# Kernel tuning notes

Hardware: AMD Instinct MI355X
Metric: run time of the kernel (lower is better)

Reference implementation:

```python
import jax, jax.numpy as jnp
import numpy as np

D_MODEL, D_K, D_V, H = 64, 32, 32, 8
B, HH, WW = 2, 48, 48
NQ = HH * WW


def setup_inputs() -> dict:
    key = jax.random.key(0)
    ks = jax.random.split(key, 16)
    inp = {
        "queries": jax.random.normal(ks[0], (B, D_MODEL, HH, WW), jnp.float32),
        "keys": jax.random.normal(ks[1], (B, D_MODEL, HH, WW), jnp.float32),
        "values": jax.random.normal(ks[2], (B, D_MODEL, HH, WW), jnp.float32),
        "attention_weights": jax.random.uniform(ks[3], (B, H, NQ, NQ), jnp.float32),
        "attention_mask": jax.random.randint(ks[4], (B, H, NQ, NQ), 0, 2) > 0,
        # Linear params: torch init normal(std=0.001) weights, zero bias
        "Wq": 0.001 * jax.random.normal(ks[5], (H * D_K, D_MODEL), jnp.float32),
        "bq": jnp.zeros((H * D_K,), jnp.float32),
        "Wk": 0.001 * jax.random.normal(ks[6], (H * D_K, D_MODEL), jnp.float32),
        "bk": jnp.zeros((H * D_K,), jnp.float32),
        "Wv": 0.001 * jax.random.normal(ks[7], (H * D_V, D_MODEL), jnp.float32),
        "bv": jnp.zeros((H * D_V,), jnp.float32),
        "Wo": 0.001 * jax.random.normal(ks[8], (D_MODEL, H * D_V), jnp.float32),
        "bo": jnp.zeros((D_MODEL,), jnp.float32),
    }
    return inp


def reference(queries, keys, values, attention_weights, attention_mask,
              Wq, bq, Wk, bk, Wv, bv, Wo, bo):
    b, c, hh, ww = queries.shape
    nq = hh * ww
    # torch .view(b, -1, c) on contiguous (b,c,h,w) is a raw row-major reshape
    qf = queries.reshape(b, nq, c)
    kf = keys.reshape(b, nq, c)
    vf = values.reshape(b, nq, c)
    q = (qf @ Wq.T + bq).reshape(b, nq, H, D_K).transpose(0, 2, 1, 3)  # b h nq dk
    k = (kf @ Wk.T + bk).reshape(b, nq, H, D_K).transpose(0, 2, 1, 3)  # b h nk dk
    v = (vf @ Wv.T + bv).reshape(b, nq, H, D_V).transpose(0, 2, 1, 3)  # b h nk dv
    att = jnp.einsum('bhqd,bhkd->bhqk', q, k) / np.sqrt(D_K).astype(np.float32)
    att = att * attention_weights
    att = jnp.where(attention_mask, -jnp.inf, att)
    att = jax.nn.softmax(att, axis=-1)  # dropout is identity in eval mode
    out = jnp.einsum('bhqk,bhkd->bhqd', att, v)
    out = out.transpose(0, 2, 1, 3).reshape(b, nq, H * D_V)
    out = out @ Wo.T + bo  # (b, nq, d_model)
    return out.reshape(b, -1, hh, ww)  # (b, d_model, h, w)
```

## Files before the change

### kernel.cpp

```cpp
#include <hip/hip_runtime.h>


typedef __attribute__((ext_vector_type(8))) short bf16x8;
typedef __attribute__((ext_vector_type(4))) short bf16x4;
typedef __attribute__((ext_vector_type(4))) float f32x4;
typedef __attribute__((ext_vector_type(4))) unsigned int u32x4;

constexpr int B_  = 2;
constexpr int H_  = 8;
constexpr int NQ_ = 2304;
constexpr int DM_ = 64;
constexpr int DK_ = 32;
constexpr int NT_ = NQ_ / 32;
constexpr int CH_ = 3;
constexpr int TPC_ = NT_ / CH_;
constexpr int GT_ = B_ * H_ * (NQ_ / 16);
constexpr float SCALE_ = 0.17677669529663687f;

constexpr size_t OFF_Q    = 0;
constexpr size_t OFF_K    = 2359296;
constexpr size_t OFF_V    = 4718592;
constexpr size_t OFF_OMID = 7077888;
constexpr size_t OFF_FLAG = 11796480;
constexpr size_t OFF_OP   = 11796736;
constexpr size_t OFF_ML   = 25952512;

static __device__ __forceinline__ unsigned short f2bf(float f) {
    unsigned int u = __builtin_bit_cast(unsigned int, f);
    u += 0x7fffu + ((u >> 16) & 1u);
    return (unsigned short)(u >> 16);
}

__global__ void detect_mask_k(const unsigned int* __restrict__ m, int* __restrict__ flag) {
    int t = threadIdx.x;
    unsigned int v = 0;
    for (int k = 0; k < 16; ++k) v |= m[t * 16 + k];
    unsigned long long b = __ballot(v > 1u);
    if (t == 0) *flag = (b != 0ull) ? 1 : 0;
}

__global__ __launch_bounds__(256) void proj_qkv_k(
    const float* __restrict__ qin, const float* __restrict__ kin, const float* __restrict__ vin,
    const float* __restrict__ Wq, const float* __restrict__ bq,
    const float* __restrict__ Wk, const float* __restrict__ bk,
    const float* __restrict__ Wv, const float* __restrict__ bv,
    unsigned short* __restrict__ Qbf, unsigned short* __restrict__ Kbf,
    unsigned short* __restrict__ Vbf)
{
    const int sel = blockIdx.y;
    const float* in  = sel == 0 ? qin : (sel == 1 ? kin : vin);
    const float* W   = sel == 0 ? Wq  : (sel == 1 ? Wk  : Wv);
    const float* bia = sel == 0 ? bq  : (sel == 1 ? bk  : bv);

    const int rt = blockIdx.x;
    const int b  = rt / (NQ_ / 8);
    const int r0 = (rt % (NQ_ / 8)) * 8;

    __shared__ alignas(16) float ins[8][64];
    const int t = threadIdx.x;
    const float4* src = reinterpret_cast<const float4*>(in + ((size_t)b * NQ_ + r0) * DM_);
    if (t < 128) reinterpret_cast<float4*>(&ins[0][0])[t] = src[t];
    __syncthreads();

    float acc[8];
#pragma unroll
    for (int r = 0; r < 8; ++r) acc[r] = 0.f;
    const float* wrow = W + t * DM_;
    for (int m = 0; m < DM_; ++m) {
        float wv = wrow[m];
#pragma unroll
        for (int r = 0; r < 8; ++r) acc[r] += ins[r][m] * wv;
    }
    const float bb = bia[t];
    const int h = t >> 5, d = t & 31;
#pragma unroll
    for (int r = 0; r < 8; ++r) {
        float o = acc[r] + bb;
        if (sel == 0) o *= SCALE_;
        unsigned short bvv = f2bf(o);
        if (sel == 2) Vbf[(((size_t)b * H_ + h) * DK_ + d) * NQ_ + (r0 + r)] = bvv;
        else {
            unsigned short* out = (sel == 1) ? Kbf : Qbf;
            out[(((size_t)b * H_ + h) * NQ_ + (r0 + r)) * DK_ + d] = bvv;
        }
    }
}

struct Slot {
    bf16x8 ka0, ka1;
    f32x4  w0, w1;
    bf16x4 v00, v01, v10, v11;
};
template<bool ISBYTE> struct MaskSlot;
template<> struct MaskSlot<true>  { unsigned int a, b; };
template<> struct MaskSlot<false> { u32x4 a, b; };

template<bool ISBYTE>
static __device__ __forceinline__ void issue_slot(
    Slot& s, MaskSlot<ISBYTE>& ms,
    const unsigned short* __restrict__ kbase, const unsigned short* __restrict__ vbase,
    const float* __restrict__ wrow, const unsigned char* __restrict__ mrowp,
    int j0, int l15, int hi)
{
    s.ka0 = *reinterpret_cast<const bf16x8*>(kbase + (size_t)(j0 + l15) * DK_ + 8 * hi);
    s.ka1 = *reinterpret_cast<const bf16x8*>(kbase + (size_t)(j0 + 16 + l15) * DK_ + 8 * hi);
    s.w0  = *reinterpret_cast<const f32x4*>(wrow + j0 + 4 * hi);
    s.w1  = *reinterpret_cast<const f32x4*>(wrow + j0 + 16 + 4 * hi);
    if constexpr (ISBYTE) {
        ms.a = *reinterpret_cast<const unsigned int*>(mrowp + j0 + 4 * hi);
        ms.b = *reinterpret_cast<const unsigned int*>(mrowp + j0 + 16 + 4 * hi);
    } else {
        ms.a = *reinterpret_cast<const u32x4*>(mrowp + (size_t)(j0 + 4 * hi) * 4);
        ms.b = *reinterpret_cast<const u32x4*>(mrowp + (size_t)(j0 + 16 + 4 * hi) * 4);
    }
    s.v00 = *reinterpret_cast<const bf16x4*>(vbase + (size_t)l15 * NQ_ + j0 + 4 * hi);
    s.v01 = *reinterpret_cast<const bf16x4*>(vbase + (size_t)l15 * NQ_ + j0 + 16 + 4 * hi);
    s.v10 = *reinterpret_cast<const bf16x4*>(vbase + (size_t)(16 + l15) * NQ_ + j0 + 4 * hi);
    s.v11 = *reinterpret_cast<const bf16x4*>(vbase + (size_t)(16 + l15) * NQ_ + j0 + 16 + 4 * hi);
}

template<bool ISBYTE>
static __device__ __forceinline__ void consume_slot(
    const Slot& s, const MaskSlot<ISBYTE>& ms, bf16x8 qb,
    f32x4& oacc0, f32x4& oacc1, float& lrun)
{
    const f32x4 zero = {0.f, 0.f, 0.f, 0.f};
    f32x4 s0 = __builtin_amdgcn_mfma_f32_16x16x32_bf16(s.ka0, qb, zero, 0, 0, 0);
    f32x4 s1 = __builtin_amdgcn_mfma_f32_16x16x32_bf16(s.ka1, qb, zero, 0, 0, 0);

    unsigned int ba, bb;
    if constexpr (ISBYTE) { ba = ms.a; bb = ms.b; }
    else {
        ba = (ms.a[0] & 1u) | ((ms.a[1] & 1u) << 8) | ((ms.a[2] & 1u) << 16) | ((ms.a[3] & 1u) << 24);
        bb = (ms.b[0] & 1u) | ((ms.b[1] & 1u) << 8) | ((ms.b[2] & 1u) << 16) | ((ms.b[3] & 1u) << 24);
    }

    float p0[4], p1[4];
#pragma unroll
    for (int r = 0; r < 4; ++r) {
        float e0 = __expf(s0[r] * s.w0[r]);
        float e1 = __expf(s1[r] * s.w1[r]);
        p0[r] = ((ba >> (8 * r)) & 0xffu) ? 0.f : e0;
        p1[r] = ((bb >> (8 * r)) & 0xffu) ? 0.f : e1;
    }
    lrun += ((p0[0] + p0[1]) + (p0[2] + p0[3])) + ((p1[0] + p1[1]) + (p1[2] + p1[3]));

    bf16x8 pa;
#pragma unroll
    for (int r = 0; r < 4; ++r) {
        pa[r]     = (short)f2bf(p0[r]);
        pa[4 + r] = (short)f2bf(p1[r]);
    }
    bf16x8 vb0 = __builtin_shufflevector(s.v00, s.v01, 0, 1, 2, 3, 4, 5, 6, 7);
    bf16x8 vb1 = __builtin_shufflevector(s.v10, s.v11, 0, 1, 2, 3, 4, 5, 6, 7);
    oacc0 = __builtin_amdgcn_mfma_f32_16x16x32_bf16(pa, vb0, oacc0, 0, 0, 0);
    oacc1 = __builtin_amdgcn_mfma_f32_16x16x32_bf16(pa, vb1, oacc1, 0, 0, 0);
}

template<bool ISBYTE>
__global__ __launch_bounds__(256) void attn_k(
    const unsigned short* __restrict__ Qbf,
    const unsigned short* __restrict__ Kbf,
    const unsigned short* __restrict__ Vbf,
    const float* __restrict__ attw,
    const unsigned char* __restrict__ maskb,
    const int* __restrict__ flagp,
    float* __restrict__ Opart,
    float* __restrict__ MLpart)
{
    if (((*flagp) != 0) != ISBYTE) return;

    const int lane = threadIdx.x & 63;
    const int l15 = lane & 15, hi = lane >> 4;
    const int g = blockIdx.x * 4 + (threadIdx.x >> 6);
    const int chunk = blockIdx.y;
    const int bh = g / (NQ_ / 16);
    const int it = g % (NQ_ / 16);
    const int i0 = it * 16;

    const unsigned short* qbase = Qbf + (size_t)bh * NQ_ * DK_;
    const unsigned short* kbase = Kbf + (size_t)bh * NQ_ * DK_;
    const unsigned short* vbase = Vbf + (size_t)bh * DK_ * NQ_;

    const int q = i0 + l15;
    bf16x8 qb = *reinterpret_cast<const bf16x8*>(qbase + (size_t)q * DK_ + 8 * hi);

    const float* wrow = attw + ((size_t)bh * NQ_ + q) * NQ_;
    const unsigned char* mrowp = maskb + ((size_t)bh * NQ_ + q) * NQ_ * (ISBYTE ? 1 : 4);

    f32x4 oacc0 = {0.f, 0.f, 0.f, 0.f}, oacc1 = {0.f, 0.f, 0.f, 0.f};
    float lrun = 0.f;

    const int t0 = chunk * TPC_, t1 = t0 + TPC_;

    Slot sl0, sl1, sl2;
    MaskSlot<ISBYTE> ms0, ms1, ms2;
    issue_slot<ISBYTE>(sl0, ms0, kbase, vbase, wrow, mrowp, t0 * 32, l15, hi);
    issue_slot<ISBYTE>(sl1, ms1, kbase, vbase, wrow, mrowp, (t0 + 1) * 32, l15, hi);
    issue_slot<ISBYTE>(sl2, ms2, kbase, vbase, wrow, mrowp, (t0 + 2) * 32, l15, hi);

    for (int tt = t0; tt < t1; tt += 3) {
        consume_slot<ISBYTE>(sl0, ms0, qb, oacc0, oacc1, lrun);
        if (tt + 3 < t1)
            issue_slot<ISBYTE>(sl0, ms0, kbase, vbase, wrow, mrowp, (tt + 3) * 32, l15, hi);
        consume_slot<ISBYTE>(sl1, ms1, qb, oacc0, oacc1, lrun);
        if (tt + 4 < t1)
            issue_slot<ISBYTE>(sl1, ms1, kbase, vbase, wrow, mrowp, (tt + 4) * 32, l15, hi);
        consume_slot<ISBYTE>(sl2, ms2, qb, oacc0, oacc1, lrun);
        if (tt + 5 < t1)
            issue_slot<ISBYTE>(sl2, ms2, kbase, vbase, wrow, mrowp, (tt + 5) * 32, l15, hi);
    }

    float* op = Opart + ((size_t)chunk * GT_ + g) * 512;
#pragma unroll
    for (int r = 0; r < 4; ++r) {
        op[(4 * hi + r) * 32 + l15]      = oacc0[r];
        op[(4 * hi + r) * 32 + 16 + l15] = oacc1[r];
    }
    lrun += __shfl_xor(lrun, 16, 64);
    lrun += __shfl_xor(lrun, 32, 64);
    if (hi == 0) {
        float* mlp = MLpart + ((size_t)chunk * GT_ + g) * 32;
        mlp[l15] = lrun;
    }
}

__global__ __launch_bounds__(64) void combine_k(
    const float* __restrict__ Opart, const float* __restrict__ MLpart,
    float* __restrict__ Omid)
{
    const int g = blockIdx.x;
    const int lane = threadIdx.x;
    const int row = lane >> 2;
    const int c4  = (lane & 3) * 8;
    const int bh = g / (NQ_ / 16);
    const int it = g % (NQ_ / 16);
    const int b = bh / H_, h = bh % H_;

    float lg = 0.f;
#pragma unroll
    for (int c = 0; c < CH_; ++c)
        lg += MLpart[((size_t)c * GT_ + g) * 32 + row];
    float inv = 1.0f / lg;

    const size_t ob = (size_t)row * 32 + c4;
    f32x4 a0 = {0.f,0.f,0.f,0.f}, a1 = {0.f,0.f,0.f,0.f};
#pragma unroll
    for (int c = 0; c < CH_; ++c) {
        const float* opp = Opart + ((size_t)c * GT_ + g) * 512 + ob;
        a0 += *reinterpret_cast<const f32x4*>(opp);
        a1 += *reinterpret_cast<const f32x4*>(opp + 4);
    }
    a0 *= inv; a1 *= inv;
    float* dst = Omid + ((size_t)b * NQ_ + it * 16 + row) * 256 + h * 32 + c4;
    *reinterpret_cast<f32x4*>(dst)     = a0;
    *reinterpret_cast<f32x4*>(dst + 4) = a1;
}

__global__ __launch_bounds__(256) void proj_out_k(
    const float* __restrict__ Omid, const float* __restrict__ Wo,
    const float* __restrict__ bo, float* __restrict__ out)
{
    const int rt = blockIdx.x;
    const int b  = rt / (NQ_ / 16);
    const int r0 = (rt % (NQ_ / 16)) * 16;

    __shared__ alignas(16) float lds[16][256];
    const int t = threadIdx.x;
    const float4* src = reinterpret_cast<const float4*>(Omid + ((size_t)b * NQ_ + r0) * 256);
#pragma unroll
    for (int k = 0; k < 4; ++k) reinterpret_cast<float4*>(&lds[0][0])[t + k * 256] = src[t + k * 256];
    __syncthreads();

    const int m = t & 63, rg = t >> 6;
    float acc[4] = {0.f, 0.f, 0.f, 0.f};
    const float* wrow = Wo + m * 256;
    for (int c = 0; c < 256; ++c) {
        float wv = wrow[c];
#pragma unroll
        for (int rr = 0; rr < 4; ++rr) acc[rr] += lds[rg * 4 + rr][c] * wv;
    }
    const float bb = bo[m];
#pragma unroll
    for (int rr = 0; rr < 4; ++rr)
        out[((size_t)b * NQ_ + r0 + rg * 4 + rr) * 64 + m] = acc[rr] + bb;
}

extern "C" void kernel_launch(void* const* d_in, const int* in_sizes, int n_in,
                              void* d_out, int out_size, void* d_ws, size_t ws_size,
                              hipStream_t stream)
{
    (void)in_sizes; (void)n_in; (void)out_size; (void)ws_size;
    const float* qin  = (const float*)d_in[0];
    const float* kin  = (const float*)d_in[1];
    const float* vin  = (const float*)d_in[2];
    const float* attw = (const float*)d_in[3];
    const void*  mask = d_in[4];
    const float* Wq = (const float*)d_in[5];
    const float* bq = (const float*)d_in[6];
    const float* Wk = (const float*)d_in[7];
    const float* bk = (const float*)d_in[8];
    const float* Wv = (const float*)d_in[9];
    const float* bv = (const float*)d_in[10];
    const float* Wo = (const float*)d_in[11];
    const float* bo = (const float*)d_in[12];

    char* ws = (char*)d_ws;
    unsigned short* Qbf   = (unsigned short*)(ws + OFF_Q);
    unsigned short* Kbf   = (unsigned short*)(ws + OFF_K);
    unsigned short* Vbf   = (unsigned short*)(ws + OFF_V);
    float*          Omid  = (float*)(ws + OFF_OMID);
    int*            flag  = (int*)(ws + OFF_FLAG);
    float*          Opart = (float*)(ws + OFF_OP);
    float*          MLp   = (float*)(ws + OFF_ML);

    detect_mask_k<<<1, 64, 0, stream>>>((const unsigned int*)mask, flag);
    proj_qkv_k<<<dim3(B_ * NQ_ / 8, 3), 256, 0, stream>>>(
        qin, kin, vin, Wq, bq, Wk, bk, Wv, bv, Qbf, Kbf, Vbf);
    attn_k<true><<<dim3(GT_ / 4, CH_), 256, 0, stream>>>(
        Qbf, Kbf, Vbf, attw, (const unsigned char*)mask, flag, Opart, MLp);
    attn_k<false><<<dim3(GT_ / 4, CH_), 256, 0, stream>>>(
        Qbf, Kbf, Vbf, attw, (const unsigned char*)mask, flag, Opart, MLp);
    combine_k<<<GT_, 64, 0, stream>>>(Opart, MLp, Omid);
    proj_out_k<<<B_ * NQ_ / 16, 256, 0, stream>>>(Omid, Wo, bo, (float*)d_out);
}
```

Baseline: 241.4 us.

## Prefetch attention weights and mask in 4-tile spans, separate from K/V pipeline

Restructures the attention streaming loop so the dominant attention-weight and mask loads are fetched in larger 4-tile spans, double-buffered (WA/WB, MA/MB) well ahead of use. K/V loads move to their own two-slot ring. The two mask variants are also split into separate kernels with different launch_bounds occupancy hints (3 and 2 blocks per CU). The aim is more memory-level parallelism on the bandwidth-bound weight/mask stream. The cost is higher register pressure, and the loop now hardcodes 24 tiles per chunk.

```diff
diff --git a/kernel.cpp b/kernel.cpp
--- a/kernel.cpp
+++ b/kernel.cpp
@@ -86,60 +86,71 @@
     }
 }
 
-struct Slot {
+struct KVSlot {
     bf16x8 ka0, ka1;
-    f32x4  w0, w1;
     bf16x4 v00, v01, v10, v11;
 };
-template<bool ISBYTE> struct MaskSlot;
-template<> struct MaskSlot<true>  { unsigned int a, b; };
-template<> struct MaskSlot<false> { u32x4 a, b; };
-
-template<bool ISBYTE>
-static __device__ __forceinline__ void issue_slot(
-    Slot& s, MaskSlot<ISBYTE>& ms,
+
+static __device__ __forceinline__ void issue_kv(KVSlot& s,
     const unsigned short* __restrict__ kbase, const unsigned short* __restrict__ vbase,
-    const float* __restrict__ wrow, const unsigned char* __restrict__ mrowp,
     int j0, int l15, int hi)
 {
     s.ka0 = *reinterpret_cast<const bf16x8*>(kbase + (size_t)(j0 + l15) * DK_ + 8 * hi);
     s.ka1 = *reinterpret_cast<const bf16x8*>(kbase + (size_t)(j0 + 16 + l15) * DK_ + 8 * hi);
-    s.w0  = *reinterpret_cast<const f32x4*>(wrow + j0 + 4 * hi);
-    s.w1  = *reinterpret_cast<const f32x4*>(wrow + j0 + 16 + 4 * hi);
-    if constexpr (ISBYTE) {
-        ms.a = *reinterpret_cast<const unsigned int*>(mrowp + j0 + 4 * hi);
-        ms.b = *reinterpret_cast<const unsigned int*>(mrowp + j0 + 16 + 4 * hi);
-    } else {
-        ms.a = *reinterpret_cast<const u32x4*>(mrowp + (size_t)(j0 + 4 * hi) * 4);
-        ms.b = *reinterpret_cast<const u32x4*>(mrowp + (size_t)(j0 + 16 + 4 * hi) * 4);
-    }
     s.v00 = *reinterpret_cast<const bf16x4*>(vbase + (size_t)l15 * NQ_ + j0 + 4 * hi);
     s.v01 = *reinterpret_cast<const bf16x4*>(vbase + (size_t)l15 * NQ_ + j0 + 16 + 4 * hi);
     s.v10 = *reinterpret_cast<const bf16x4*>(vbase + (size_t)(16 + l15) * NQ_ + j0 + 4 * hi);
     s.v11 = *reinterpret_cast<const bf16x4*>(vbase + (size_t)(16 + l15) * NQ_ + j0 + 16 + 4 * hi);
 }
 
-template<bool ISBYTE>
-static __device__ __forceinline__ void consume_slot(
-    const Slot& s, const MaskSlot<ISBYTE>& ms, bf16x8 qb,
+template<bool ISBYTE> struct MSpan;
+template<> struct MSpan<true>  { unsigned int m[8]; };
+template<> struct MSpan<false> { u32x4 m[8]; };
+
+static __device__ __forceinline__ void loadW(f32x4 (&W)[8], const float* __restrict__ p) {
+#pragma unroll
+    for (int u = 0; u < 4; ++u) {
+        W[2 * u]     = *reinterpret_cast<const f32x4*>(p + 32 * u);
+        W[2 * u + 1] = *reinterpret_cast<const f32x4*>(p + 32 * u + 16);
+    }
+}
+
+static __device__ __forceinline__ void loadM(MSpan<true>& M, const unsigned char* __restrict__ p) {
+#pragma unroll
+    for (int u = 0; u < 4; ++u) {
+        M.m[2 * u]     = *reinterpret_cast<const unsigned int*>(p + 32 * u);
+        M.m[2 * u + 1] = *reinterpret_cast<const unsigned int*>(p + 32 * u + 16);
+    }
+}
+static __device__ __forceinline__ void loadM(MSpan<false>& M, const unsigned char* __restrict__ p) {
+#pragma unroll
+    for (int u = 0; u < 4; ++u) {
+        M.m[2 * u]     = *reinterpret_cast<const u32x4*>(p + 128 * u);
+        M.m[2 * u + 1] = *reinterpret_cast<const u32x4*>(p + 128 * u + 64);
+    }
+}
+
+static __device__ __forceinline__ unsigned int mb32(unsigned int v) { return v; }
+static __device__ __forceinline__ unsigned int mb32(u32x4 v) {
+    return (v[0] & 1u) | ((v[1] & 1u) << 8) | ((v[2] & 1u) << 16) | ((v[3] & 1u) << 24);
+}
+
+template<typename MT>
+static __device__ __forceinline__ void consume_tile(
+    const KVSlot& s, f32x4 w0, f32x4 w1, MT m0r, MT m1r, bf16x8 qb,
     f32x4& oacc0, f32x4& oacc1, float& lrun)
 {
     const f32x4 zero = {0.f, 0.f, 0.f, 0.f};
     f32x4 s0 = __builtin_amdgcn_mfma_f32_16x16x32_bf16(s.ka0, qb, zero, 0, 0, 0);
     f32x4 s1 = __builtin_amdgcn_mfma_f32_16x16x32_bf16(s.ka1, qb, zero, 0, 0, 0);
 
-    unsigned int ba, bb;
-    if constexpr (ISBYTE) { ba = ms.a; bb = ms.b; }
-    else {
-        ba = (ms.a[0] & 1u) | ((ms.a[1] & 1u) << 8) | ((ms.a[2] & 1u) << 16) | ((ms.a[3] & 1u) << 24);
-        bb = (ms.b[0] & 1u) | ((ms.b[1] & 1u) << 8) | ((ms.b[2] & 1u) << 16) | ((ms.b[3] & 1u) << 24);
-    }
+    const unsigned int ba = mb32(m0r), bb = mb32(m1r);
 
     float p0[4], p1[4];
 #pragma unroll
     for (int r = 0; r < 4; ++r) {
-        float e0 = __expf(s0[r] * s.w0[r]);
-        float e1 = __expf(s1[r] * s.w1[r]);
+        float e0 = __expf(s0[r] * w0[r]);
+        float e1 = __expf(s1[r] * w1[r]);
         p0[r] = ((ba >> (8 * r)) & 0xffu) ? 0.f : e0;
         p1[r] = ((bb >> (8 * r)) & 0xffu) ? 0.f : e1;
     }
@@ -158,7 +169,24 @@
 }
 
 template<bool ISBYTE>
-__global__ __launch_bounds__(256) void attn_k(
+static __device__ __forceinline__ void consume4(
+    KVSlot& sA, KVSlot& sB, const f32x4 (&W)[8], const MSpan<ISBYTE>& M,
+    int tb, int t1,
+    const unsigned short* __restrict__ kbase, const unsigned short* __restrict__ vbase,
+    int l15, int hi, bf16x8 qb, f32x4& o0, f32x4& o1, float& lr)
+{
+    consume_tile(sA, W[0], W[1], M.m[0], M.m[1], qb, o0, o1, lr);
+    if (tb + 2 < t1) issue_kv(sA, kbase, vbase, (tb + 2) * 32, l15, hi);
+    consume_tile(sB, W[2], W[3], M.m[2], M.m[3], qb, o0, o1, lr);
+    if (tb + 3 < t1) issue_kv(sB, kbase, vbase, (tb + 3) * 32, l15, hi);
+    consume_tile(sA, W[4], W[5], M.m[4], M.m[5], qb, o0, o1, lr);
+    if (tb + 4 < t1) issue_kv(sA, kbase, vbase, (tb + 4) * 32, l15, hi);
+    consume_tile(sB, W[6], W[7], M.m[6], M.m[7], qb, o0, o1, lr);
+    if (tb + 5 < t1) issue_kv(sB, kbase, vbase, (tb + 5) * 32, l15, hi);
+}
+
+template<bool ISBYTE>
+static __device__ __forceinline__ void attn_body(
     const unsigned short* __restrict__ Qbf,
     const unsigned short* __restrict__ Kbf,
     const unsigned short* __restrict__ Vbf,
@@ -185,30 +213,38 @@
     const int q = i0 + l15;
     bf16x8 qb = *reinterpret_cast<const bf16x8*>(qbase + (size_t)q * DK_ + 8 * hi);
 
-    const float* wrow = attw + ((size_t)bh * NQ_ + q) * NQ_;
-    const unsigned char* mrowp = maskb + ((size_t)bh * NQ_ + q) * NQ_ * (ISBYTE ? 1 : 4);
+    const float* wl = attw + ((size_t)bh * NQ_ + q) * NQ_ + 4 * hi;
+    const unsigned char* ml = maskb + (((size_t)bh * NQ_ + q) * NQ_ + 4 * hi) * (ISBYTE ? 1 : 4);
+
+    const int t0 = chunk * TPC_, t1 = t0 + TPC_;
+    const size_t msc = ISBYTE ? 1 : 4;
+
+    f32x4 WA[8], WB[8];
+    MSpan<ISBYTE> MA, MB;
+    KVSlot sA, sB;
+
+    loadW(WA, wl + (size_t)t0 * 32);
+    loadM(MA, ml + (size_t)t0 * 32 * msc);
+    loadW(WB, wl + (size_t)t0 * 32 + 128);
+    loadM(MB, ml + ((size_t)t0 * 32 + 128) * msc);
+    issue_kv(sA, kbase, vbase, t0 * 32, l15, hi);
+    issue_kv(sB, kbase, vbase, t0 * 32 + 32, l15, hi);
 
     f32x4 oacc0 = {0.f, 0.f, 0.f, 0.f}, oacc1 = {0.f, 0.f, 0.f, 0.f};
     float lrun = 0.f;
 
-    const int t0 = chunk * TPC_, t1 = t0 + TPC_;
-
-    Slot sl0, sl1, sl2;
-    MaskSlot<ISBYTE> ms0, ms1, ms2;
-    issue_slot<ISBYTE>(sl0, ms0, kbase, vbase, wrow, mrowp, t0 * 32, l15, hi);
-    issue_slot<ISBYTE>(sl1, ms1, kbase, vbase, wrow, mrowp, (t0 + 1) * 32, l15, hi);
-    issue_slot<ISBYTE>(sl2, ms2, kbase, vbase, wrow, mrowp, (t0 + 2) * 32, l15, hi);
-
-    for (int tt = t0; tt < t1; tt += 3) {
-        consume_slot<ISBYTE>(sl0, ms0, qb, oacc0, oacc1, lrun);
-        if (tt + 3 < t1)
-            issue_slot<ISBYTE>(sl0, ms0, kbase, vbase, wrow, mrowp, (tt + 3) * 32, l15, hi);
-        consume_slot<ISBYTE>(sl1, ms1, qb, oacc0, oacc1, lrun);
-        if (tt + 4 < t1)
-            issue_slot<ISBYTE>(sl1, ms1, kbase, vbase, wrow, mrowp, (tt + 4) * 32, l15, hi);
-        consume_slot<ISBYTE>(sl2, ms2, qb, oacc0, oacc1, lrun);
-        if (tt + 5 < t1)
-            issue_slot<ISBYTE>(sl2, ms2, kbase, vbase, wrow, mrowp, (tt + 5) * 32, l15, hi);
+    for (int sp = 0; sp < 3; ++sp) {
+        const int tb = t0 + 8 * sp;
+        consume4<ISBYTE>(sA, sB, WA, MA, tb, t1, kbase, vbase, l15, hi, qb, oacc0, oacc1, lrun);
+        if (sp < 2) {
+            loadW(WA, wl + (size_t)(tb + 8) * 32);
+            loadM(MA, ml + (size_t)(tb + 8) * 32 * msc);
+        }
+        consume4<ISBYTE>(sA, sB, WB, MB, tb + 4, t1, kbase, vbase, l15, hi, qb, oacc0, oacc1, lrun);
+        if (sp < 2) {
+            loadW(WB, wl + (size_t)(tb + 12) * 32);
+            loadM(MB, ml + (size_t)(tb + 12) * 32 * msc);
+        }
     }
 
     float* op = Opart + ((size_t)chunk * GT_ + g) * 512;
@@ -223,6 +259,24 @@
         float* mlp = MLpart + ((size_t)chunk * GT_ + g) * 32;
         mlp[l15] = lrun;
     }
+}
+
+__global__ __launch_bounds__(256, 3) void attn_byte_k(
+    const unsigned short* __restrict__ Qbf, const unsigned short* __restrict__ Kbf,
+    const unsigned short* __restrict__ Vbf, const float* __restrict__ attw,
+    const unsigned char* __restrict__ maskb, const int* __restrict__ flagp,
+    float* __restrict__ Opart, float* __restrict__ MLpart)
+{
+    attn_body<true>(Qbf, Kbf, Vbf, attw, maskb, flagp, Opart, MLpart);
+}
+
+__global__ __launch_bounds__(256, 2) void attn_int_k(
+    const unsigned short* __restrict__ Qbf, const unsigned short* __restrict__ Kbf,
+    const unsigned short* __restrict__ Vbf, const float* __restrict__ attw,
+    const unsigned char* __restrict__ maskb, const int* __restrict__ flagp,
+    float* __restrict__ Opart, float* __restrict__ MLpart)
+{
+    attn_body<false>(Qbf, Kbf, Vbf, attw, maskb, flagp, Opart, MLpart);
 }
 
 __global__ __launch_bounds__(64) void combine_k(
@@ -317,9 +371,9 @@
     detect_mask_k<<<1, 64, 0, stream>>>((const unsigned int*)mask, flag);
     proj_qkv_k<<<dim3(B_ * NQ_ / 8, 3), 256, 0, stream>>>(
         qin, kin, vin, Wq, bq, Wk, bk, Wv, bv, Qbf, Kbf, Vbf);
-    attn_k<true><<<dim3(GT_ / 4, CH_), 256, 0, stream>>>(
+    attn_byte_k<<<dim3(GT_ / 4, CH_), 256, 0, stream>>>(
         Qbf, Kbf, Vbf, attw, (const unsigned char*)mask, flag, Opart, MLp);
-    attn_k<false><<<dim3(GT_ / 4, CH_), 256, 0, stream>>>(
+    attn_int_k<<<dim3(GT_ / 4, CH_), 256, 0, stream>>>(
         Qbf, Kbf, Vbf, attw, (const unsigned char*)mask, flag, Opart, MLp);
     combine_k<<<GT_, 64, 0, stream>>>(Opart, MLp, Omid);
     proj_out_k<<<B_ * NQ_ / 16, 256, 0, stream>>>(Omid, Wo, bo, (float*)d_out);
```

New measurement: 241.0 us. No clear change (-0.1%).

## Stage attention weight, mask, K and V tiles into LDS via async global-to-LDS loads

Applied to the files above, without the earlier changes.

The attention kernel now copies the attention-weight rows, int mask rows, K and V tiles straight from global memory into per-wave XOR-swizzled LDS buffers with global_load_lds. It double-buffers them and uses explicit vmcnt waits, replacing the old three-slot register prefetch. Blocks shrink from four waves to three so the grid divides evenly, and each wave gets 16 KB of LDS. The aim is coalesced row-wise streaming of the large weight and mask tensors with less register pressure. The cost is hand-counted waitcnt values and swizzle indexing that must match the load count exactly.

```diff
diff --git a/kernel.cpp b/kernel.cpp
--- a/kernel.cpp
+++ b/kernel.cpp
@@ -31,6 +31,10 @@
     return (unsigned short)(u >> 16);
 }
 
+#define GLL16(SRC, DST) __builtin_amdgcn_global_load_lds( \
+    (const __attribute__((address_space(1))) unsigned int*)(const void*)(SRC), \
+    (__attribute__((address_space(3))) unsigned int*)(void*)(DST), 16, 0, 0)
+
 __global__ void detect_mask_k(const unsigned int* __restrict__ m, int* __restrict__ flag) {
     int t = threadIdx.x;
     unsigned int v = 0;
@@ -86,79 +90,16 @@
     }
 }
 
-struct Slot {
+
+struct Frag {
+    f32x4 w0, w1;
+    u32x4 m0, m1;
     bf16x8 ka0, ka1;
-    f32x4  w0, w1;
     bf16x4 v00, v01, v10, v11;
 };
-template<bool ISBYTE> struct MaskSlot;
-template<> struct MaskSlot<true>  { unsigned int a, b; };
-template<> struct MaskSlot<false> { u32x4 a, b; };
 
 template<bool ISBYTE>
-static __device__ __forceinline__ void issue_slot(
-    Slot& s, MaskSlot<ISBYTE>& ms,
-    const unsigned short* __restrict__ kbase, const unsigned short* __restrict__ vbase,
-    const float* __restrict__ wrow, const unsigned char* __restrict__ mrowp,
-    int j0, int l15, int hi)
-{
-    s.ka0 = *reinterpret_cast<const bf16x8*>(kbase + (size_t)(j0 + l15) * DK_ + 8 * hi);
-    s.ka1 = *reinterpret_cast<const bf16x8*>(kbase + (size_t)(j0 + 16 + l15) * DK_ + 8 * hi);
-    s.w0  = *reinterpret_cast<const f32x4*>(wrow + j0 + 4 * hi);
-    s.w1  = *reinterpret_cast<const f32x4*>(wrow + j0 + 16 + 4 * hi);
-    if constexpr (ISBYTE) {
-        ms.a = *reinterpret_cast<const unsigned int*>(mrowp + j0 + 4 * hi);
-        ms.b = *reinterpret_cast<const unsigned int*>(mrowp + j0 + 16 + 4 * hi);
-    } else {
-        ms.a = *reinterpret_cast<const u32x4*>(mrowp + (size_t)(j0 + 4 * hi) * 4);
-        ms.b = *reinterpret_cast<const u32x4*>(mrowp + (size_t)(j0 + 16 + 4 * hi) * 4);
-    }
-    s.v00 = *reinterpret_cast<const bf16x4*>(vbase + (size_t)l15 * NQ_ + j0 + 4 * hi);
-    s.v01 = *reinterpret_cast<const bf16x4*>(vbase + (size_t)l15 * NQ_ + j0 + 16 + 4 * hi);
-    s.v10 = *reinterpret_cast<const bf16x4*>(vbase + (size_t)(16 + l15) * NQ_ + j0 + 4 * hi);
-    s.v11 = *reinterpret_cast<const bf16x4*>(vbase + (size_t)(16 + l15) * NQ_ + j0 + 16 + 4 * hi);
-}
-
-template<bool ISBYTE>
-static __device__ __forceinline__ void consume_slot(
-    const Slot& s, const MaskSlot<ISBYTE>& ms, bf16x8 qb,
-    f32x4& oacc0, f32x4& oacc1, float& lrun)
-{
-    const f32x4 zero = {0.f, 0.f, 0.f, 0.f};
-    f32x4 s0 = __builtin_amdgcn_mfma_f32_16x16x32_bf16(s.ka0, qb, zero, 0, 0, 0);
-    f32x4 s1 = __builtin_amdgcn_mfma_f32_16x16x32_bf16(s.ka1, qb, zero, 0, 0, 0);
-
-    unsigned int ba, bb;
-    if constexpr (ISBYTE) { ba = ms.a; bb = ms.b; }
-    else {
-        ba = (ms.a[0] & 1u) | ((ms.a[1] & 1u) << 8) | ((ms.a[2] & 1u) << 16) | ((ms.a[3] & 1u) << 24);
-        bb = (ms.b[0] & 1u) | ((ms.b[1] & 1u) << 8) | ((ms.b[2] & 1u) << 16) | ((ms.b[3] & 1u) << 24);
-    }
-
-    float p0[4], p1[4];
-#pragma unroll
-    for (int r = 0; r < 4; ++r) {
-        float e0 = __expf(s0[r] * s.w0[r]);
-        float e1 = __expf(s1[r] * s.w1[r]);
-        p0[r] = ((ba >> (8 * r)) & 0xffu) ? 0.f : e0;
-        p1[r] = ((bb >> (8 * r)) & 0xffu) ? 0.f : e1;
-    }
-    lrun += ((p0[0] + p0[1]) + (p0[2] + p0[3])) + ((p1[0] + p1[1]) + (p1[2] + p1[3]));
-
-    bf16x8 pa;
-#pragma unroll
-    for (int r = 0; r < 4; ++r) {
-        pa[r]     = (short)f2bf(p0[r]);
-        pa[4 + r] = (short)f2bf(p1[r]);
-    }
-    bf16x8 vb0 = __builtin_shufflevector(s.v00, s.v01, 0, 1, 2, 3, 4, 5, 6, 7);
-    bf16x8 vb1 = __builtin_shufflevector(s.v10, s.v11, 0, 1, 2, 3, 4, 5, 6, 7);
-    oacc0 = __builtin_amdgcn_mfma_f32_16x16x32_bf16(pa, vb0, oacc0, 0, 0, 0);
-    oacc1 = __builtin_amdgcn_mfma_f32_16x16x32_bf16(pa, vb1, oacc1, 0, 0, 0);
-}
-
-template<bool ISBYTE>
-__global__ __launch_bounds__(256) void attn_k(
+static __device__ __forceinline__ void attn_body(
     const unsigned short* __restrict__ Qbf,
     const unsigned short* __restrict__ Kbf,
     const unsigned short* __restrict__ Vbf,
@@ -166,49 +107,152 @@
     const unsigned char* __restrict__ maskb,
     const int* __restrict__ flagp,
     float* __restrict__ Opart,
-    float* __restrict__ MLpart)
+    float* __restrict__ MLpart,
+    char* lds)
 {
     if (((*flagp) != 0) != ISBYTE) return;
 
-    const int lane = threadIdx.x & 63;
+    const int tid = threadIdx.x;
+    const int wid = tid >> 6, lane = tid & 63;
     const int l15 = lane & 15, hi = lane >> 4;
-    const int g = blockIdx.x * 4 + (threadIdx.x >> 6);
+    const int g = blockIdx.x * 3 + wid;
     const int chunk = blockIdx.y;
     const int bh = g / (NQ_ / 16);
     const int it = g % (NQ_ / 16);
     const int i0 = it * 16;
+    const int q = i0 + l15;
 
     const unsigned short* qbase = Qbf + (size_t)bh * NQ_ * DK_;
     const unsigned short* kbase = Kbf + (size_t)bh * NQ_ * DK_;
     const unsigned short* vbase = Vbf + (size_t)bh * DK_ * NQ_;
-
-    const int q = i0 + l15;
+    const float* wbase = attw + (size_t)bh * NQ_ * NQ_;
+
     bf16x8 qb = *reinterpret_cast<const bf16x8*>(qbase + (size_t)q * DK_ + 8 * hi);
 
-    const float* wrow = attw + ((size_t)bh * NQ_ + q) * NQ_;
-    const unsigned char* mrowp = maskb + ((size_t)bh * NQ_ + q) * NQ_ * (ISBYTE ? 1 : 4);
+    const int r8 = lane >> 3, q8 = lane & 7;
+    const int wq = (q8 ^ r8) * 4;
+    const float* pW0 = wbase + (size_t)(i0 + r8) * NQ_ + wq;
+    const float* pW1 = pW0 + (size_t)8 * NQ_;
+    const int* pM0 = (const int*)maskb + (size_t)(bh * NQ_ + i0 + r8) * NQ_ + wq;
+    const int* pM1 = pM0 + (size_t)8 * NQ_;
+    const int r4 = lane >> 2, q4 = lane & 3;
+    const int kq = (q4 ^ ((r4 >> 1) & 3)) * 8;
+    const unsigned short* pK0 = kbase + (size_t)r4 * DK_ + kq;
+    const unsigned short* pK1 = pK0 + (size_t)16 * DK_;
+    const unsigned short* pV0 = vbase + (size_t)r4 * NQ_ + kq;
+    const unsigned short* pV1 = pV0 + (size_t)16 * NQ_;
+
+    const unsigned char* mrow = maskb + ((size_t)bh * NQ_ + q) * NQ_;
+
+    char* sb0 = lds + wid * 16384;
+    char* sb1 = sb0 + 8192;
+
+    auto stage = [&](char* sb, int tile) {
+        const int j0 = tile * 32;
+        GLL16(pW0 + j0, sb);
+        GLL16(pW1 + j0, sb + 1024);
+        if constexpr (!ISBYTE) {
+            GLL16(pM0 + j0, sb + 2048);
+            GLL16(pM1 + j0, sb + 3072);
+        }
+        GLL16(pK0 + (size_t)j0 * DK_, sb + 4096);
+        GLL16(pK1 + (size_t)j0 * DK_, sb + 5120);
+        GLL16(pV0 + j0, sb + 6144);
+        GLL16(pV1 + j0, sb + 7168);
+    };
+
+    auto load_frag = [&](const char* sb, Frag& f) {
+        const int qA = (hi ^ (l15 & 7)) << 4;
+        const int qB = ((hi + 4) ^ (l15 & 7)) << 4;
+        const int rw = l15 << 7;
+        f.w0 = *(const f32x4*)(sb + rw + qA);
+        f.w1 = *(const f32x4*)(sb + rw + qB);
+        if constexpr (!ISBYTE) {
+            f.m0 = *(const u32x4*)(sb + 2048 + rw + qA);
+            f.m1 = *(const u32x4*)(sb + 2048 + rw + qB);
+        }
+        const int kc = (hi ^ ((l15 >> 1) & 3)) << 4;
+        f.ka0 = *(const bf16x8*)(sb + 4096 + (l15 << 6) + kc);
+        f.ka1 = *(const bf16x8*)(sb + 4096 + ((16 + l15) << 6) + kc);
+        const int vh = (hi & 1) << 3;
+        const int vc0 = ((((hi >> 1)) ^ ((l15 >> 1) & 3)) << 4) + vh;
+        const int vc1 = (((2 + (hi >> 1)) ^ ((l15 >> 1) & 3)) << 4) + vh;
+        f.v00 = *(const bf16x4*)(sb + 6144 + (l15 << 6) + vc0);
+        f.v01 = *(const bf16x4*)(sb + 6144 + (l15 << 6) + vc1);
+        f.v10 = *(const bf16x4*)(sb + 6144 + ((16 + l15) << 6) + vc0);
+        f.v11 = *(const bf16x4*)(sb + 6144 + ((16 + l15) << 6) + vc1);
+    };
 
     f32x4 oacc0 = {0.f, 0.f, 0.f, 0.f}, oacc1 = {0.f, 0.f, 0.f, 0.f};
     float lrun = 0.f;
 
+    auto compute_frag = [&](const Frag& f, unsigned int mba, unsigned int mbb) {
+        const f32x4 zero = {0.f, 0.f, 0.f, 0.f};
+        f32x4 s0 = __builtin_amdgcn_mfma_f32_16x16x32_bf16(f.ka0, qb, zero, 0, 0, 0);
+        f32x4 s1 = __builtin_amdgcn_mfma_f32_16x16x32_bf16(f.ka1, qb, zero, 0, 0, 0);
+        float p0[4], p1[4];
+#pragma unroll
+        for (int r = 0; r < 4; ++r) {
+            float e0 = __expf(s0[r] * f.w0[r]);
+            float e1 = __expf(s1[r] * f.w1[r]);
+            bool k0, k1;
+            if constexpr (ISBYTE) {
+                k0 = ((mba >> (8 * r)) & 0xffu) != 0;
+                k1 = ((mbb >> (8 * r)) & 0xffu) != 0;
+            } else {
+                k0 = f.m0[r] != 0;
+                k1 = f.m1[r] != 0;
+            }
+            p0[r] = k0 ? 0.f : e0;
+            p1[r] = k1 ? 0.f : e1;
+        }
+        lrun += ((p0[0] + p0[1]) + (p0[2] + p0[3])) + ((p1[0] + p1[1]) + (p1[2] + p1[3]));
+        bf16x8 pa;
+#pragma unroll
+        for (int r = 0; r < 4; ++r) {
+            pa[r]     = (short)f2bf(p0[r]);
+            pa[4 + r] = (short)f2bf(p1[r]);
+        }
+        bf16x8 vb0 = __builtin_shufflevector(f.v00, f.v01, 0, 1, 2, 3, 4, 5, 6, 7);
+        bf16x8 vb1 = __builtin_shufflevector(f.v10, f.v11, 0, 1, 2, 3, 4, 5, 6, 7);
+        oacc0 = __builtin_amdgcn_mfma_f32_16x16x32_bf16(pa, vb0, oacc0, 0, 0, 0);
+        oacc1 = __builtin_amdgcn_mfma_f32_16x16x32_bf16(pa, vb1, oacc1, 0, 0, 0);
+    };
+
     const int t0 = chunk * TPC_, t1 = t0 + TPC_;
 
-    Slot sl0, sl1, sl2;
-    MaskSlot<ISBYTE> ms0, ms1, ms2;
-    issue_slot<ISBYTE>(sl0, ms0, kbase, vbase, wrow, mrowp, t0 * 32, l15, hi);
-    issue_slot<ISBYTE>(sl1, ms1, kbase, vbase, wrow, mrowp, (t0 + 1) * 32, l15, hi);
-    issue_slot<ISBYTE>(sl2, ms2, kbase, vbase, wrow, mrowp, (t0 + 2) * 32, l15, hi);
-
-    for (int tt = t0; tt < t1; tt += 3) {
-        consume_slot<ISBYTE>(sl0, ms0, qb, oacc0, oacc1, lrun);
-        if (tt + 3 < t1)
-            issue_slot<ISBYTE>(sl0, ms0, kbase, vbase, wrow, mrowp, (tt + 3) * 32, l15, hi);
-        consume_slot<ISBYTE>(sl1, ms1, qb, oacc0, oacc1, lrun);
-        if (tt + 4 < t1)
-            issue_slot<ISBYTE>(sl1, ms1, kbase, vbase, wrow, mrowp, (tt + 4) * 32, l15, hi);
-        consume_slot<ISBYTE>(sl2, ms2, qb, oacc0, oacc1, lrun);
-        if (tt + 5 < t1)
-            issue_slot<ISBYTE>(sl2, ms2, kbase, vbase, wrow, mrowp, (tt + 5) * 32, l15, hi);
+    stage(sb0, t0);
+    stage(sb1, t0 + 1);
+    int cur = 0;
+
+    for (int u = t0; u < t1 - 1; ++u) {
+        char* sbc = cur ? sb1 : sb0;
+        if constexpr (ISBYTE) asm volatile("s_waitcnt vmcnt(6)" ::: "memory");
+        else                  asm volatile("s_waitcnt vmcnt(8)" ::: "memory");
+        Frag f;
+        load_frag(sbc, f);
+        unsigned int mba = 0, mbb = 0;
+        if constexpr (ISBYTE) {
+            mba = *(const unsigned int*)(mrow + u * 32 + 4 * hi);
+            mbb = *(const unsigned int*)(mrow + u * 32 + 16 + 4 * hi);
+        }
+        asm volatile("s_waitcnt lgkmcnt(0)" ::: "memory");
+        if (u + 2 < t1) stage(sbc, u + 2);
+        compute_frag(f, mba, mbb);
+        cur ^= 1;
+    }
+    {
+        char* sbc = cur ? sb1 : sb0;
+        asm volatile("s_waitcnt vmcnt(0)" ::: "memory");
+        Frag f;
+        load_frag(sbc, f);
+        unsigned int mba = 0, mbb = 0;
+        if constexpr (ISBYTE) {
+            mba = *(const unsigned int*)(mrow + (t1 - 1) * 32 + 4 * hi);
+            mbb = *(const unsigned int*)(mrow + (t1 - 1) * 32 + 16 + 4 * hi);
+        }
+        asm volatile("s_waitcnt lgkmcnt(0)" ::: "memory");
+        compute_frag(f, mba, mbb);
     }
 
     float* op = Opart + ((size_t)chunk * GT_ + g) * 512;
@@ -223,6 +267,26 @@
         float* mlp = MLpart + ((size_t)chunk * GT_ + g) * 32;
         mlp[l15] = lrun;
     }
+}
+
+__global__ __launch_bounds__(192) void attn_byte_k(
+    const unsigned short* __restrict__ Qbf, const unsigned short* __restrict__ Kbf,
+    const unsigned short* __restrict__ Vbf, const float* __restrict__ attw,
+    const unsigned char* __restrict__ maskb, const int* __restrict__ flagp,
+    float* __restrict__ Opart, float* __restrict__ MLpart)
+{
+    __shared__ alignas(16) char lds[3 * 2 * 8192];
+    attn_body<true>(Qbf, Kbf, Vbf, attw, maskb, flagp, Opart, MLpart, lds);
+}
+
+__global__ __launch_bounds__(192) void attn_int_k(
+    const unsigned short* __restrict__ Qbf, const unsigned short* __restrict__ Kbf,
+    const unsigned short* __restrict__ Vbf, const float* __restrict__ attw,
+    const unsigned char* __restrict__ maskb, const int* __restrict__ flagp,
+    float* __restrict__ Opart, float* __restrict__ MLpart)
+{
+    __shared__ alignas(16) char lds[3 * 2 * 8192];
+    attn_body<false>(Qbf, Kbf, Vbf, attw, maskb, flagp, Opart, MLpart, lds);
 }
 
 __global__ __launch_bounds__(64) void combine_k(
@@ -317,9 +381,9 @@
     detect_mask_k<<<1, 64, 0, stream>>>((const unsigned int*)mask, flag);
     proj_qkv_k<<<dim3(B_ * NQ_ / 8, 3), 256, 0, stream>>>(
         qin, kin, vin, Wq, bq, Wk, bk, Wv, bv, Qbf, Kbf, Vbf);
-    attn_k<true><<<dim3(GT_ / 4, CH_), 256, 0, stream>>>(
+    attn_byte_k<<<dim3(GT_ / 3, CH_), 192, 0, stream>>>(
         Qbf, Kbf, Vbf, attw, (const unsigned char*)mask, flag, Opart, MLp);
-    attn_k<false><<<dim3(GT_ / 4, CH_), 256, 0, stream>>>(
+    attn_int_k<<<dim3(GT_ / 3, CH_), 192, 0, stream>>>(
         Qbf, Kbf, Vbf, attw, (const unsigned char*)mask, flag, Opart, MLp);
     combine_k<<<GT_, 64, 0, stream>>>(Opart, MLp, Omid);
     proj_out_k<<<B_ * NQ_ / 16, 256, 0, stream>>>(Omid, Wo, bo, (float*)d_out);
```

Measured after the change: 217.9 us (median of 2 runs). 1.11x faster.

## Prepack attention weights and mask into bf16 MFMA-layout buffer per chunk

Applied to the files above, without the earlier changes.

Adds a prepack kernel that reads the fp32 attention weights and the mask for one key chunk through shared memory and writes a single bf16 value per element, laid out in MFMA lane order. A masked position is encoded as -1, which is safe because the weights are non-negative. The attention kernel then loads one 16-byte vector per slot instead of separate weight and mask loads. The cost is an extra write and re-read of the packed buffer, more kernel launches (two prepack and one attention launch per chunk), and bf16 rounding of the weights.

```diff
diff --git a/kernel.cpp b/kernel.cpp
--- a/kernel.cpp
+++ b/kernel.cpp
@@ -24,11 +24,15 @@
 constexpr size_t OFF_FLAG = 11796480;
 constexpr size_t OFF_OP   = 11796736;
 constexpr size_t OFF_ML   = 25952512;
+constexpr size_t OFF_PK   = 26837248;
 
 static __device__ __forceinline__ unsigned short f2bf(float f) {
     unsigned int u = __builtin_bit_cast(unsigned int, f);
     u += 0x7fffu + ((u >> 16) & 1u);
     return (unsigned short)(u >> 16);
+}
+static __device__ __forceinline__ float bf2f(short s) {
+    return __builtin_bit_cast(float, ((unsigned int)(unsigned short)s) << 16);
 }
 
 __global__ void detect_mask_k(const unsigned int* __restrict__ m, int* __restrict__ flag) {
@@ -86,62 +90,113 @@
     }
 }
 
+template<bool ISBYTE>
+static __device__ __forceinline__ void prepack_body(
+    const float* __restrict__ attw, const unsigned char* __restrict__ maskb,
+    const int* __restrict__ flagp, unsigned short* __restrict__ packed, int chunk)
+{
+    if (((*flagp) != 0) != ISBYTE) return;
+
+    const int g = blockIdx.x;
+    const int bh = g / 144, it = g % 144;
+    const int i0 = it * 16;
+    const int t = threadIdx.x;
+
+    __shared__ float Wl[16][260];
+    __shared__ int   Ml[16][260];
+
+    const size_t rowbase = ((size_t)bh * NQ_ + i0) * NQ_;
+    const int cchunk = chunk * (TPC_ * 32);
+    unsigned short* pout = packed + (size_t)g * (TPC_ * 512);
+
+    for (int sp = 0; sp < 3; ++sp) {
+        const int c0 = cchunk + sp * 256;
+#pragma unroll
+        for (int k = 0; k < 4; ++k) {
+            const int i = t + k * 256;
+            const int row = i >> 6, c4 = (i & 63) * 4;
+            const size_t goff = rowbase + (size_t)row * NQ_ + c0 + c4;
+            float4 wv = *reinterpret_cast<const float4*>(attw + goff);
+            *reinterpret_cast<float4*>(&Wl[row][c4]) = wv;
+            if constexpr (ISBYTE) {
+                uchar4 mv = *reinterpret_cast<const uchar4*>(maskb + goff);
+                int4 mi = {mv.x, mv.y, mv.z, mv.w};
+                *reinterpret_cast<int4*>(&Ml[row][c4]) = mi;
+            } else {
+                int4 mi = *reinterpret_cast<const int4*>((const int*)maskb + goff);
+                *reinterpret_cast<int4*>(&Ml[row][c4]) = mi;
+            }
+        }
+        __syncthreads();
+#pragma unroll
+        for (int sidx = 0; sidx < 2; ++sidx) {
+            const int s = t + sidx * 256;
+            const int jloc = s >> 6, l = s & 63;
+            const int l15 = l & 15, hi = l >> 4;
+            const int cb = jloc * 32 + 4 * hi;
+            unsigned short u[8];
+#pragma unroll
+            for (int i2 = 0; i2 < 4; ++i2) {
+                u[i2]     = Ml[l15][cb + i2]      ? (unsigned short)0xBF80u : f2bf(Wl[l15][cb + i2]);
+                u[4 + i2] = Ml[l15][cb + 16 + i2] ? (unsigned short)0xBF80u : f2bf(Wl[l15][cb + 16 + i2]);
+            }
+            u32x4 o;
+#pragma unroll
+            for (int k = 0; k < 4; ++k)
+                o[k] = (unsigned int)u[2 * k] | ((unsigned int)u[2 * k + 1] << 16);
+            *reinterpret_cast<u32x4*>(pout + ((size_t)(sp * 8 + jloc)) * 512 + l * 8) = o;
+        }
+        __syncthreads();
+    }
+}
+
+__global__ __launch_bounds__(256) void prepack_byte_k(
+    const float* __restrict__ attw, const unsigned char* __restrict__ maskb,
+    const int* __restrict__ flagp, unsigned short* __restrict__ packed, int chunk)
+{ prepack_body<true>(attw, maskb, flagp, packed, chunk); }
+
+__global__ __launch_bounds__(256) void prepack_int_k(
+    const float* __restrict__ attw, const unsigned char* __restrict__ maskb,
+    const int* __restrict__ flagp, unsigned short* __restrict__ packed, int chunk)
+{ prepack_body<false>(attw, maskb, flagp, packed, chunk); }
+
 struct Slot {
+    bf16x8 wm;
     bf16x8 ka0, ka1;
-    f32x4  w0, w1;
     bf16x4 v00, v01, v10, v11;
 };
-template<bool ISBYTE> struct MaskSlot;
-template<> struct MaskSlot<true>  { unsigned int a, b; };
-template<> struct MaskSlot<false> { u32x4 a, b; };
-
-template<bool ISBYTE>
+
 static __device__ __forceinline__ void issue_slot(
-    Slot& s, MaskSlot<ISBYTE>& ms,
+    Slot& s, const unsigned short* __restrict__ pwm,
     const unsigned short* __restrict__ kbase, const unsigned short* __restrict__ vbase,
-    const float* __restrict__ wrow, const unsigned char* __restrict__ mrowp,
-    int j0, int l15, int hi)
-{
+    int u, int j0base, int lane, int l15, int hi)
+{
+    const int j0 = j0base + u * 32;
+    s.wm  = *reinterpret_cast<const bf16x8*>(pwm + (size_t)u * 512 + lane * 8);
     s.ka0 = *reinterpret_cast<const bf16x8*>(kbase + (size_t)(j0 + l15) * DK_ + 8 * hi);
     s.ka1 = *reinterpret_cast<const bf16x8*>(kbase + (size_t)(j0 + 16 + l15) * DK_ + 8 * hi);
-    s.w0  = *reinterpret_cast<const f32x4*>(wrow + j0 + 4 * hi);
-    s.w1  = *reinterpret_cast<const f32x4*>(wrow + j0 + 16 + 4 * hi);
-    if constexpr (ISBYTE) {
-        ms.a = *reinterpret_cast<const unsigned int*>(mrowp + j0 + 4 * hi);
-        ms.b = *reinterpret_cast<const unsigned int*>(mrowp + j0 + 16 + 4 * hi);
-    } else {
-        ms.a = *reinterpret_cast<const u32x4*>(mrowp + (size_t)(j0 + 4 * hi) * 4);
-        ms.b = *reinterpret_cast<const u32x4*>(mrowp + (size_t)(j0 + 16 + 4 * hi) * 4);
-    }
     s.v00 = *reinterpret_cast<const bf16x4*>(vbase + (size_t)l15 * NQ_ + j0 + 4 * hi);
     s.v01 = *reinterpret_cast<const bf16x4*>(vbase + (size_t)l15 * NQ_ + j0 + 16 + 4 * hi);
     s.v10 = *reinterpret_cast<const bf16x4*>(vbase + (size_t)(16 + l15) * NQ_ + j0 + 4 * hi);
     s.v11 = *reinterpret_cast<const bf16x4*>(vbase + (size_t)(16 + l15) * NQ_ + j0 + 16 + 4 * hi);
 }
 
-template<bool ISBYTE>
 static __device__ __forceinline__ void consume_slot(
-    const Slot& s, const MaskSlot<ISBYTE>& ms, bf16x8 qb,
-    f32x4& oacc0, f32x4& oacc1, float& lrun)
+    const Slot& s, bf16x8 qb, f32x4& oacc0, f32x4& oacc1, float& lrun)
 {
     const f32x4 zero = {0.f, 0.f, 0.f, 0.f};
     f32x4 s0 = __builtin_amdgcn_mfma_f32_16x16x32_bf16(s.ka0, qb, zero, 0, 0, 0);
     f32x4 s1 = __builtin_amdgcn_mfma_f32_16x16x32_bf16(s.ka1, qb, zero, 0, 0, 0);
 
-    unsigned int ba, bb;
-    if constexpr (ISBYTE) { ba = ms.a; bb = ms.b; }
-    else {
-        ba = (ms.a[0] & 1u) | ((ms.a[1] & 1u) << 8) | ((ms.a[2] & 1u) << 16) | ((ms.a[3] & 1u) << 24);
-        bb = (ms.b[0] & 1u) | ((ms.b[1] & 1u) << 8) | ((ms.b[2] & 1u) << 16) | ((ms.b[3] & 1u) << 24);
-    }
-
     float p0[4], p1[4];
 #pragma unroll
     for (int r = 0; r < 4; ++r) {
-        float e0 = __expf(s0[r] * s.w0[r]);
-        float e1 = __expf(s1[r] * s.w1[r]);
-        p0[r] = ((ba >> (8 * r)) & 0xffu) ? 0.f : e0;
-        p1[r] = ((bb >> (8 * r)) & 0xffu) ? 0.f : e1;
+        float w0f = bf2f(s.wm[r]);
+        float w1f = bf2f(s.wm[4 + r]);
+        float e0 = __expf(s0[r] * w0f);
+        float e1 = __expf(s1[r] * w1f);
+        p0[r] = (w0f < 0.f) ? 0.f : e0;
+        p1[r] = (w1f < 0.f) ? 0.f : e1;
     }
     lrun += ((p0[0] + p0[1]) + (p0[2] + p0[3])) + ((p1[0] + p1[1]) + (p1[2] + p1[3]));
 
@@ -157,23 +212,18 @@
     oacc1 = __builtin_amdgcn_mfma_f32_16x16x32_bf16(pa, vb1, oacc1, 0, 0, 0);
 }
 
-template<bool ISBYTE>
 __global__ __launch_bounds__(256) void attn_k(
     const unsigned short* __restrict__ Qbf,
     const unsigned short* __restrict__ Kbf,
     const unsigned short* __restrict__ Vbf,
-    const float* __restrict__ attw,
-    const unsigned char* __restrict__ maskb,
-    const int* __restrict__ flagp,
+    const unsigned short* __restrict__ packed,
     float* __restrict__ Opart,
-    float* __restrict__ MLpart)
-{
-    if (((*flagp) != 0) != ISBYTE) return;
-
+    float* __restrict__ MLpart,
+    int chunk)
+{
     const int lane = threadIdx.x & 63;
     const int l15 = lane & 15, hi = lane >> 4;
     const int g = blockIdx.x * 4 + (threadIdx.x >> 6);
-    const int chunk = blockIdx.y;
     const int bh = g / (NQ_ / 16);
     const int it = g % (NQ_ / 16);
     const int i0 = it * 16;
@@ -181,34 +231,28 @@
     const unsigned short* qbase = Qbf + (size_t)bh * NQ_ * DK_;
     const unsigned short* kbase = Kbf + (size_t)bh * NQ_ * DK_;
     const unsigned short* vbase = Vbf + (size_t)bh * DK_ * NQ_;
+    const unsigned short* pwm   = packed + (size_t)g * (TPC_ * 512);
 
     const int q = i0 + l15;
     bf16x8 qb = *reinterpret_cast<const bf16x8*>(qbase + (size_t)q * DK_ + 8 * hi);
 
-    const float* wrow = attw + ((size_t)bh * NQ_ + q) * NQ_;
-    const unsigned char* mrowp = maskb + ((size_t)bh * NQ_ + q) * NQ_ * (ISBYTE ? 1 : 4);
+    const int j0base = chunk * TPC_ * 32;
 
     f32x4 oacc0 = {0.f, 0.f, 0.f, 0.f}, oacc1 = {0.f, 0.f, 0.f, 0.f};
     float lrun = 0.f;
 
-    const int t0 = chunk * TPC_, t1 = t0 + TPC_;
-
     Slot sl0, sl1, sl2;
-    MaskSlot<ISBYTE> ms0, ms1, ms2;
-    issue_slot<ISBYTE>(sl0, ms0, kbase, vbase, wrow, mrowp, t0 * 32, l15, hi);
-    issue_slot<ISBYTE>(sl1, ms1, kbase, vbase, wrow, mrowp, (t0 + 1) * 32, l15, hi);
-    issue_slot<ISBYTE>(sl2, ms2, kbase, vbase, wrow, mrowp, (t0 + 2) * 32, l15, hi);
-
-    for (int tt = t0; tt < t1; tt += 3) {
-        consume_slot<ISBYTE>(sl0, ms0, qb, oacc0, oacc1, lrun);
-        if (tt + 3 < t1)
-            issue_slot<ISBYTE>(sl0, ms0, kbase, vbase, wrow, mrowp, (tt + 3) * 32, l15, hi);
-        consume_slot<ISBYTE>(sl1, ms1, qb, oacc0, oacc1, lrun);
-        if (tt + 4 < t1)
-            issue_slot<ISBYTE>(sl1, ms1, kbase, vbase, wrow, mrowp, (tt + 4) * 32, l15, hi);
-        consume_slot<ISBYTE>(sl2, ms2, qb, oacc0, oacc1, lrun);
-        if (tt + 5 < t1)
-            issue_slot<ISBYTE>(sl2, ms2, kbase, vbase, wrow, mrowp, (tt + 5) * 32, l15, hi);
+    issue_slot(sl0, pwm, kbase, vbase, 0, j0base, lane, l15, hi);
+    issue_slot(sl1, pwm, kbase, vbase, 1, j0base, lane, l15, hi);
+    issue_slot(sl2, pwm, kbase, vbase, 2, j0base, lane, l15, hi);
+
+    for (int u = 0; u < TPC_; u += 3) {
+        consume_slot(sl0, qb, oacc0, oacc1, lrun);
+        if (u + 3 < TPC_) issue_slot(sl0, pwm, kbase, vbase, u + 3, j0base, lane, l15, hi);
+        consume_slot(sl1, qb, oacc0, oacc1, lrun);
+        if (u + 4 < TPC_) issue_slot(sl1, pwm, kbase, vbase, u + 4, j0base, lane, l15, hi);
+        consume_slot(sl2, qb, oacc0, oacc1, lrun);
+        if (u + 5 < TPC_) issue_slot(sl2, pwm, kbase, vbase, u + 5, j0base, lane, l15, hi);
     }
 
     float* op = Opart + ((size_t)chunk * GT_ + g) * 512;
@@ -313,14 +357,18 @@
     int*            flag  = (int*)(ws + OFF_FLAG);
     float*          Opart = (float*)(ws + OFF_OP);
     float*          MLp   = (float*)(ws + OFF_ML);
+    unsigned short* Pk    = (unsigned short*)(ws + OFF_PK);
 
     detect_mask_k<<<1, 64, 0, stream>>>((const unsigned int*)mask, flag);
     proj_qkv_k<<<dim3(B_ * NQ_ / 8, 3), 256, 0, stream>>>(
         qin, kin, vin, Wq, bq, Wk, bk, Wv, bv, Qbf, Kbf, Vbf);
-    attn_k<true><<<dim3(GT_ / 4, CH_), 256, 0, stream>>>(
-        Qbf, Kbf, Vbf, attw, (const unsigned char*)mask, flag, Opart, MLp);
-    attn_k<false><<<dim3(GT_ / 4, CH_), 256, 0, stream>>>(
-        Qbf, Kbf, Vbf, attw, (const unsigned char*)mask, flag, Opart, MLp);
+    for (int c = 0; c < CH_; ++c) {
+        prepack_byte_k<<<GT_, 256, 0, stream>>>(
+            attw, (const unsigned char*)mask, flag, Pk, c);
+        prepack_int_k<<<GT_, 256, 0, stream>>>(
+            attw, (const unsigned char*)mask, flag, Pk, c);
+        attn_k<<<GT_ / 4, 256, 0, stream>>>(Qbf, Kbf, Vbf, Pk, Opart, MLp, c);
+    }
     combine_k<<<GT_, 64, 0, stream>>>(Opart, MLp, Omid);
     proj_out_k<<<B_ * NQ_ / 16, 256, 0, stream>>>(Omid, Wo, bo, (float*)d_out);
 }
```

Result: slower. 362.3 us (+50.1%).
